# Kernel tuning notes

Measured on AMD Instinct MI355X. Metric: run time of the kernel, lower is better.

## Reference

```python
import jax, jax.numpy as jnp
import numpy as np
from jax import lax

WINDOW_SIZE = 11
SIGMA = 1.5
CHANNELS = 1


def _make_window(ws, channels):
    # matches torch: exp(-(x - ws/2)^2 / (2*sigma^2)), note center at ws/2 (not (ws-1)/2)
    x = np.arange(ws, dtype=np.float64)
    g = np.exp(-(x - ws / 2) ** 2 / (2.0 * SIGMA ** 2))
    g = g / g.sum()
    w2 = np.outer(g, g).astype(np.float32)  # [ws, ws]
    w = np.broadcast_to(w2, (channels, 1, ws, ws)).copy()  # OIHW depthwise
    return jnp.asarray(w)


def _dwconv(x, w, channels):
    pad = (WINDOW_SIZE - 1) // 2
    return lax.conv_general_dilated(
        x, w, window_strides=(1, 1), padding=[(pad, pad), (pad, pad)],
        dimension_numbers=("NCHW", "OIHW", "NCHW"), feature_group_count=channels)


def setup_inputs() -> dict:
    key = jax.random.key(0)
    k1, k2 = jax.random.split(key)
    img1 = jax.random.normal(k1, (32, 1, 512, 512), dtype=jnp.float32)
    img2 = jax.random.normal(k2, (32, 1, 512, 512), dtype=jnp.float32)
    return {"img1": img1, "img2": img2}


def reference(img1, img2):
    channels = img1.shape[1]
    w = _make_window(WINDOW_SIZE, channels).astype(img1.dtype)

    mu1 = _dwconv(img1, w, channels)
    mu2 = _dwconv(img2, w, channels)
    mu1_sq = mu1 * mu1
    mu2_sq = mu2 * mu2
    mu1_mu2 = mu1 * mu2
    sigma1_sq = _dwconv(img1 * img1, w, channels) - mu1_sq
    sigma2_sq = _dwconv(img2 * img2, w, channels) - mu2_sq
    sigma12 = _dwconv(img1 * img2, w, channels) - mu1_mu2

    dynamic_L = jnp.max(img1) - jnp.min(img1)
    dynamic_L = jnp.where(dynamic_L == 0, jnp.asarray(5.0, img1.dtype), dynamic_L)
    C1 = (0.01 * dynamic_L) ** 2
    C2 = (0.03 * dynamic_L) ** 2

    ssim_map = ((2 * mu1_mu2 + C1) * (2 * sigma12 + C2)) / (
        (mu1_sq + mu2_sq + C1) * (sigma1_sq + sigma2_sq + C2))
    return ssim_map
```

## Files before the change

kernel.cpp:

```cpp
#include <hip/hip_runtime.h>
#include <math.h>

#define IMG 512
#define TW 64
#define TH 16
#define RS 82
#define NQ 20
#define NV2 (8 * NQ)
#define BT 256
#define MMB 1024

struct W11 { float w[11]; };

__device__ __forceinline__ unsigned omap(float f) {
  unsigned b = __float_as_uint(f);
  return (b & 0x80000000u) ? ~b : (b | 0x80000000u);
}
__device__ __forceinline__ float ounmap(unsigned u) {
  return __uint_as_float((u & 0x80000000u) ? (u ^ 0x80000000u) : ~u);
}

__global__ __launch_bounds__(256) void minmax_part(const float4* __restrict__ img,
                                                   int n4, unsigned* __restrict__ part) {
  unsigned mx = 0u, mn = 0xFFFFFFFFu;
  int stride = gridDim.x * blockDim.x;
  for (int i = blockIdx.x * blockDim.x + threadIdx.x; i < n4; i += stride) {
    float4 v = img[i];
    unsigned a = omap(v.x), b = omap(v.y), c = omap(v.z), d = omap(v.w);
    mx = max(mx, max(max(a, b), max(c, d)));
    mn = min(mn, min(min(a, b), min(c, d)));
  }
  #pragma unroll
  for (int off = 32; off > 0; off >>= 1) {
    mx = max(mx, __shfl_down(mx, off));
    mn = min(mn, __shfl_down(mn, off));
  }
  __shared__ unsigned smx[4], smn[4];
  int lane = threadIdx.x & 63, wv = threadIdx.x >> 6;
  if (lane == 0) { smx[wv] = mx; smn[wv] = mn; }
  __syncthreads();
  if (threadIdx.x == 0) {
    mx = max(max(smx[0], smx[1]), max(smx[2], smx[3]));
    mn = min(min(smn[0], smn[1]), min(smn[2], smn[3]));
    part[2 * blockIdx.x]     = mx;
    part[2 * blockIdx.x + 1] = mn;
  }
}

__global__ __launch_bounds__(256) void minmax_final(const unsigned* __restrict__ part,
                                                    unsigned* __restrict__ ws) {
  unsigned mx = 0u, mn = 0xFFFFFFFFu;
  for (int i = threadIdx.x; i < MMB; i += 256) {
    mx = max(mx, part[2 * i]);
    mn = min(mn, part[2 * i + 1]);
  }
  #pragma unroll
  for (int off = 32; off > 0; off >>= 1) {
    mx = max(mx, __shfl_down(mx, off));
    mn = min(mn, __shfl_down(mn, off));
  }
  __shared__ unsigned smx[4], smn[4];
  int lane = threadIdx.x & 63, wv = threadIdx.x >> 6;
  if (lane == 0) { smx[wv] = mx; smn[wv] = mn; }
  __syncthreads();
  if (threadIdx.x == 0) {
    ws[0] = max(max(smx[0], smx[1]), max(smx[2], smx[3]));
    ws[1] = min(min(smn[0], smn[1]), min(smn[2], smn[3]));
  }
}

__device__ __forceinline__ void vtask2(int t, int x0, int y0, bool y_full,
                                       const float* __restrict__ p1,
                                       const float* __restrict__ p2,
                                       const W11& wv,
                                       float (*V)[TH][RS]) {
  const int p = t / NQ;
  const int q = t - p * NQ;
  const int gx0 = x0 - 8 + 4 * q;
  const int gy0 = y0 + 2 * p - 5;

  float A[4][4], B[4][4];
  #pragma unroll
  for (int f = 0; f < 4; ++f)
    #pragma unroll
    for (int c = 0; c < 4; ++c) { A[f][c] = 0.f; B[f][c] = 0.f; }

#define VSTEP2(k, a, b)                                                       \
  {                                                                           \
    float sx = a.x * a.x + b.x * b.x, sy = a.y * a.y + b.y * b.y;             \
    float sz = a.z * a.z + b.z * b.z, sw = a.w * a.w + b.w * b.w;             \
    float px = a.x * b.x, py = a.y * b.y, pz = a.z * b.z, pw = a.w * b.w;     \
    if ((k) < 11) { float w = wv.w[(k)];                                      \
      A[0][0] += w * a.x; A[0][1] += w * a.y; A[0][2] += w * a.z; A[0][3] += w * a.w; \
      A[1][0] += w * b.x; A[1][1] += w * b.y; A[1][2] += w * b.z; A[1][3] += w * b.w; \
      A[2][0] += w * sx;  A[2][1] += w * sy;  A[2][2] += w * sz;  A[2][3] += w * sw;  \
      A[3][0] += w * px;  A[3][1] += w * py;  A[3][2] += w * pz;  A[3][3] += w * pw; }\
    if ((k) > 0) { float w = wv.w[(k) - 1];                                   \
      B[0][0] += w * a.x; B[0][1] += w * a.y; B[0][2] += w * a.z; B[0][3] += w * a.w; \
      B[1][0] += w * b.x; B[1][1] += w * b.y; B[1][2] += w * b.z; B[1][3] += w * b.w; \
      B[2][0] += w * sx;  B[2][1] += w * sy;  B[2][2] += w * sz;  B[2][3] += w * sw;  \
      B[3][0] += w * px;  B[3][1] += w * py;  B[3][2] += w * pz;  B[3][3] += w * pw; }\
  }

  if ((unsigned)gx0 < IMG) {
    if (y_full) {
      const float4* Ap = (const float4*)(p1 + (size_t)gy0 * IMG + gx0);
      const float4* Bp = (const float4*)(p2 + (size_t)gy0 * IMG + gx0);
      #pragma unroll
      for (int k = 0; k < 12; ++k) {
        float4 a = Ap[k * (IMG / 4)];
        float4 b = Bp[k * (IMG / 4)];
        VSTEP2(k, a, b);
      }
    } else {
      #pragma unroll
      for (int k = 0; k < 12; ++k) {
        int row = gy0 + k;
        float4 a = make_float4(0.f, 0.f, 0.f, 0.f);
        float4 b = make_float4(0.f, 0.f, 0.f, 0.f);
        if ((unsigned)row < IMG) {
          a = *(const float4*)(p1 + (size_t)row * IMG + gx0);
          b = *(const float4*)(p2 + (size_t)row * IMG + gx0);
        }
        VSTEP2(k, a, b);
      }
    }
  }
#undef VSTEP2

  const int r0 = 2 * p;
  *(float2*)&V[0][r0][4 * q]         = make_float2(A[0][0], A[0][1]);
  *(float2*)&V[0][r0][4 * q + 2]     = make_float2(A[0][2], A[0][3]);
  *(float2*)&V[1][r0][4 * q]         = make_float2(A[1][0], A[1][1]);
  *(float2*)&V[1][r0][4 * q + 2]     = make_float2(A[1][2], A[1][3]);
  *(float2*)&V[2][r0][4 * q]         = make_float2(A[2][0], A[2][1]);
  *(float2*)&V[2][r0][4 * q + 2]     = make_float2(A[2][2], A[2][3]);
  *(float2*)&V[3][r0][4 * q]         = make_float2(A[3][0], A[3][1]);
  *(float2*)&V[3][r0][4 * q + 2]     = make_float2(A[3][2], A[3][3]);
  *(float2*)&V[0][r0 + 1][4 * q]     = make_float2(B[0][0], B[0][1]);
  *(float2*)&V[0][r0 + 1][4 * q + 2] = make_float2(B[0][2], B[0][3]);
  *(float2*)&V[1][r0 + 1][4 * q]     = make_float2(B[1][0], B[1][1]);
  *(float2*)&V[1][r0 + 1][4 * q + 2] = make_float2(B[1][2], B[1][3]);
  *(float2*)&V[2][r0 + 1][4 * q]     = make_float2(B[2][0], B[2][1]);
  *(float2*)&V[2][r0 + 1][4 * q + 2] = make_float2(B[2][2], B[2][3]);
  *(float2*)&V[3][r0 + 1][4 * q]     = make_float2(B[3][0], B[3][1]);
  *(float2*)&V[3][r0 + 1][4 * q + 2] = make_float2(B[3][2], B[3][3]);
}

__global__ __launch_bounds__(BT, 4) void ssim_k(const float* __restrict__ img1,
                                                const float* __restrict__ img2,
                                                float* __restrict__ out,
                                                const unsigned* __restrict__ ws,
                                                W11 wv) {
  __shared__ float V[4][TH][RS];

  const int tid = threadIdx.x;
  const int bx = blockIdx.x, by = blockIdx.y, n = blockIdx.z;
  const float* p1 = img1 + (size_t)n * IMG * IMG;
  const float* p2 = img2 + (size_t)n * IMG * IMG;
  const int x0 = bx * TW;
  const int y0 = by * TH;

  float L = ounmap(ws[0]) - ounmap(ws[1]);
  if (L == 0.f) L = 5.f;
  float C1 = 0.01f * L; C1 *= C1;
  float C2 = 0.03f * L; C2 *= C2;

  const bool y_full = (by > 0) & (by < IMG / TH - 1);

  if (tid < NV2) vtask2(tid, x0, y0, y_full, p1, p2, wv, V);

  __syncthreads();

  {
    const int r  = tid & 15;
    const int c4 = (tid >> 4) << 2;

    float acc[4][4];
    #pragma unroll
    for (int f = 0; f < 4; ++f)
      #pragma unroll
      for (int c = 0; c < 4; ++c) acc[f][c] = 0.f;

    float v[16];
    #pragma unroll
    for (int f = 0; f < 4; ++f) {
      const float* row = &V[f][r][c4 + 2];
      float2 g0 = *(const float2*)(row + 0);
      float2 g1 = *(const float2*)(row + 2);
      float2 g2 = *(const float2*)(row + 4);
      float2 g3 = *(const float2*)(row + 6);
      float2 g4 = *(const float2*)(row + 8);
      float2 g5 = *(const float2*)(row + 10);
      float2 g6 = *(const float2*)(row + 12);
      float2 g7 = *(const float2*)(row + 14);
      v[0]  = g0.x; v[1]  = g0.y; v[2]  = g1.x; v[3]  = g1.y;
      v[4]  = g2.x; v[5]  = g2.y; v[6]  = g3.x; v[7]  = g3.y;
      v[8]  = g4.x; v[9]  = g4.y; v[10] = g5.x; v[11] = g5.y;
      v[12] = g6.x; v[13] = g6.y; v[14] = g7.x; v[15] = g7.y;
      #pragma unroll
      for (int k = 0; k < 11; ++k) {
        float wk = wv.w[k];
        #pragma unroll
        for (int c = 0; c < 4; ++c) acc[f][c] += wk * v[c + 1 + k];
      }
    }

    float res[4];
    #pragma unroll
    for (int c = 0; c < 4; ++c) {
      float mu1 = acc[0][c], mu2 = acc[1][c];
      float mu1s = mu1 * mu1, mu2s = mu2 * mu2, mu12 = mu1 * mu2;
      float sS  = acc[2][c] - mu1s - mu2s;
      float s12 = acc[3][c] - mu12;
      float num = (2.f * mu12 + C1) * (2.f * s12 + C2);
      float den = (mu1s + mu2s + C1) * (sS + C2);
      res[c] = num / den;
    }
    float* op = out + (size_t)n * IMG * IMG + (size_t)(y0 + r) * IMG + x0 + c4;
    *(float4*)op = make_float4(res[0], res[1], res[2], res[3]);
  }
}

extern "C" void kernel_launch(void* const* d_in, const int* in_sizes, int n_in,
                              void* d_out, int out_size, void* d_ws, size_t ws_size,
                              hipStream_t stream) {
  const float* img1 = (const float*)d_in[0];
  const float* img2 = (const float*)d_in[1];
  float* out = (float*)d_out;
  unsigned* ws = (unsigned*)d_ws;
  unsigned* part = ws + 16;
  int n = in_sizes[0];
  int batch = n / (IMG * IMG);

  W11 wv;
  double g[11], s = 0.0;
  for (int i = 0; i < 11; ++i) { double d = i - 5.5; g[i] = exp(-(d * d) / 4.5); s += g[i]; }
  for (int i = 0; i < 11; ++i) wv.w[i] = (float)(g[i] / s);

  minmax_part<<<MMB, 256, 0, stream>>>((const float4*)img1, n / 4, part);
  minmax_final<<<1, 256, 0, stream>>>(part, ws);
  dim3 grid(IMG / TW, IMG / TH, batch);
  ssim_k<<<grid, BT, 0, stream>>>(img1, img2, out, ws, wv);
}
```

Baseline: 132.9 us.

## Stage input tiles in LDS with all threads and merge minmax via atomics

Every thread of the block now cooperatively loads the padded input tile for both images into a shared Raw buffer, and the vertical pass reads from LDS instead of global memory. Previously only 160 threads issued strided global loads, each covering 12 rows. The separate minmax_final kernel is replaced by atomicMax/atomicMin on the workspace, which is initialised with two memsets. This adds LDS usage and a barrier, which may lower occupancy, and swaps one kernel launch for two memset operations.

```diff
diff --git a/kernel.cpp b/kernel.cpp
--- a/kernel.cpp
+++ b/kernel.cpp
@@ -5,9 +5,11 @@
 #define TW 64
 #define TH 16
 #define RS 82
+#define RAWS 84
 #define NQ 20
 #define NV2 (8 * NQ)
 #define BT 256
+#define NCH (26 * 20)
 #define MMB 1024
 
 struct W11 { float w[11]; };
@@ -21,7 +23,7 @@
 }
 
 __global__ __launch_bounds__(256) void minmax_part(const float4* __restrict__ img,
-                                                   int n4, unsigned* __restrict__ part) {
+                                                   int n4, unsigned* __restrict__ ws) {
   unsigned mx = 0u, mn = 0xFFFFFFFFu;
   int stride = gridDim.x * blockDim.x;
   for (int i = blockIdx.x * blockDim.x + threadIdx.x; i < n4; i += stride) {
@@ -42,42 +44,16 @@
   if (threadIdx.x == 0) {
     mx = max(max(smx[0], smx[1]), max(smx[2], smx[3]));
     mn = min(min(smn[0], smn[1]), min(smn[2], smn[3]));
-    part[2 * blockIdx.x]     = mx;
-    part[2 * blockIdx.x + 1] = mn;
-  }
-}
-
-__global__ __launch_bounds__(256) void minmax_final(const unsigned* __restrict__ part,
-                                                    unsigned* __restrict__ ws) {
-  unsigned mx = 0u, mn = 0xFFFFFFFFu;
-  for (int i = threadIdx.x; i < MMB; i += 256) {
-    mx = max(mx, part[2 * i]);
-    mn = min(mn, part[2 * i + 1]);
-  }
-  #pragma unroll
-  for (int off = 32; off > 0; off >>= 1) {
-    mx = max(mx, __shfl_down(mx, off));
-    mn = min(mn, __shfl_down(mn, off));
-  }
-  __shared__ unsigned smx[4], smn[4];
-  int lane = threadIdx.x & 63, wv = threadIdx.x >> 6;
-  if (lane == 0) { smx[wv] = mx; smn[wv] = mn; }
-  __syncthreads();
-  if (threadIdx.x == 0) {
-    ws[0] = max(max(smx[0], smx[1]), max(smx[2], smx[3]));
-    ws[1] = min(min(smn[0], smn[1]), min(smn[2], smn[3]));
-  }
-}
-
-__device__ __forceinline__ void vtask2(int t, int x0, int y0, bool y_full,
-                                       const float* __restrict__ p1,
-                                       const float* __restrict__ p2,
-                                       const W11& wv,
+    atomicMax(&ws[0], mx);
+    atomicMin(&ws[1], mn);
+  }
+}
+
+__device__ __forceinline__ void vtask2(int t, const W11& wv,
+                                       const float (*Raw)[26][RAWS],
                                        float (*V)[TH][RS]) {
   const int p = t / NQ;
   const int q = t - p * NQ;
-  const int gx0 = x0 - 8 + 4 * q;
-  const int gy0 = y0 + 2 * p - 5;
 
   float A[4][4], B[4][4];
   #pragma unroll
@@ -85,8 +61,13 @@
     #pragma unroll
     for (int c = 0; c < 4; ++c) { A[f][c] = 0.f; B[f][c] = 0.f; }
 
-#define VSTEP2(k, a, b)                                                       \
+  const float* r1 = &Raw[0][2 * p][4 * q];
+  const float* r2 = &Raw[1][2 * p][4 * q];
+
+#define VSTEP2(k)                                                             \
   {                                                                           \
+    float4 a = *(const float4*)(r1 + (k) * RAWS);                             \
+    float4 b = *(const float4*)(r2 + (k) * RAWS);                             \
     float sx = a.x * a.x + b.x * b.x, sy = a.y * a.y + b.y * b.y;             \
     float sz = a.z * a.z + b.z * b.z, sw = a.w * a.w + b.w * b.w;             \
     float px = a.x * b.x, py = a.y * b.y, pz = a.z * b.z, pw = a.w * b.w;     \
@@ -102,30 +83,8 @@
       B[3][0] += w * px;  B[3][1] += w * py;  B[3][2] += w * pz;  B[3][3] += w * pw; }\
   }
 
-  if ((unsigned)gx0 < IMG) {
-    if (y_full) {
-      const float4* Ap = (const float4*)(p1 + (size_t)gy0 * IMG + gx0);
-      const float4* Bp = (const float4*)(p2 + (size_t)gy0 * IMG + gx0);
-      #pragma unroll
-      for (int k = 0; k < 12; ++k) {
-        float4 a = Ap[k * (IMG / 4)];
-        float4 b = Bp[k * (IMG / 4)];
-        VSTEP2(k, a, b);
-      }
-    } else {
-      #pragma unroll
-      for (int k = 0; k < 12; ++k) {
-        int row = gy0 + k;
-        float4 a = make_float4(0.f, 0.f, 0.f, 0.f);
-        float4 b = make_float4(0.f, 0.f, 0.f, 0.f);
-        if ((unsigned)row < IMG) {
-          a = *(const float4*)(p1 + (size_t)row * IMG + gx0);
-          b = *(const float4*)(p2 + (size_t)row * IMG + gx0);
-        }
-        VSTEP2(k, a, b);
-      }
-    }
-  }
+  VSTEP2(0)  VSTEP2(1)  VSTEP2(2)  VSTEP2(3)  VSTEP2(4)  VSTEP2(5)
+  VSTEP2(6)  VSTEP2(7)  VSTEP2(8)  VSTEP2(9)  VSTEP2(10) VSTEP2(11)
 #undef VSTEP2
 
   const int r0 = 2 * p;
@@ -152,6 +111,7 @@
                                                 float* __restrict__ out,
                                                 const unsigned* __restrict__ ws,
                                                 W11 wv) {
+  __shared__ float Raw[2][26][RAWS];
   __shared__ float V[4][TH][RS];
 
   const int tid = threadIdx.x;
@@ -166,10 +126,31 @@
   float C1 = 0.01f * L; C1 *= C1;
   float C2 = 0.03f * L; C2 *= C2;
 
-  const bool y_full = (by > 0) & (by < IMG / TH - 1);
-
-  if (tid < NV2) vtask2(tid, x0, y0, y_full, p1, p2, wv, V);
-
+  {
+    const int gx0 = x0 - 8;
+    const int gy0 = y0 - 5;
+#define STAGE(c)                                                              \
+    {                                                                         \
+      int row = (c) / 20;                                                     \
+      int qd  = (c) - row * 20;                                               \
+      int gy = gy0 + row, gx = gx0 + 4 * qd;                                  \
+      float4 a = make_float4(0.f, 0.f, 0.f, 0.f);                             \
+      float4 b = make_float4(0.f, 0.f, 0.f, 0.f);                             \
+      if (((unsigned)gy < IMG) & ((unsigned)gx < IMG)) {                      \
+        a = *(const float4*)(p1 + (size_t)gy * IMG + gx);                     \
+        b = *(const float4*)(p2 + (size_t)gy * IMG + gx);                     \
+      }                                                                       \
+      *(float4*)&Raw[0][row][4 * qd] = a;                                     \
+      *(float4*)&Raw[1][row][4 * qd] = b;                                     \
+    }
+    STAGE(tid)
+    STAGE(tid + 256)
+    if (tid < NCH - 512) STAGE(tid + 512)
+#undef STAGE
+  }
+  __syncthreads();
+
+  if (tid < NV2) vtask2(tid, wv, Raw, V);
   __syncthreads();
 
   {
@@ -229,7 +210,6 @@
   const float* img2 = (const float*)d_in[1];
   float* out = (float*)d_out;
   unsigned* ws = (unsigned*)d_ws;
-  unsigned* part = ws + 16;
   int n = in_sizes[0];
   int batch = n / (IMG * IMG);
 
@@ -238,8 +218,10 @@
   for (int i = 0; i < 11; ++i) { double d = i - 5.5; g[i] = exp(-(d * d) / 4.5); s += g[i]; }
   for (int i = 0; i < 11; ++i) wv.w[i] = (float)(g[i] / s);
 
-  minmax_part<<<MMB, 256, 0, stream>>>((const float4*)img1, n / 4, part);
-  minmax_final<<<1, 256, 0, stream>>>(part, ws);
+  hipMemsetAsync(ws, 0, 4, stream);
+  hipMemsetAsync(ws + 1, 0xFF, 4, stream);
+
+  minmax_part<<<MMB, 256, 0, stream>>>((const float4*)img1, n / 4, ws);
   dim3 grid(IMG / TW, IMG / TH, batch);
   ssim_k<<<grid, BT, 0, stream>>>(img1, img2, out, ws, wv);
 }
```

New measurement: 249.9 us. 1.88x slower.
